# Kernel tuning notes

Measured on AMD Instinct MI355X. Metric: run time of the kernel, lower is better.

## Reference

```python
import jax, jax.numpy as jnp
import numpy as np

DIM = 8          # per-head dim
EPS = 1e-15
GROUPS_PW = 192  # 3 * heads = 3 * 64


def _conv(x, w, groups=1, pad=0):
    return jax.lax.conv_general_dilated(
        x, w, window_strides=(1, 1), padding=[(pad, pad), (pad, pad)],
        dimension_numbers=('NCHW', 'OIHW', 'NCHW'), feature_group_count=groups)


def setup_inputs() -> dict:
    key = jax.random.key(0)
    k0, k1, k2, k3, k4 = jax.random.split(key, 5)
    B, C, H, W = 4, 512, 64, 64
    td = 512  # heads * dim
    x = jax.random.normal(k0, (B, C, H, W), jnp.float32)
    w_qkv = jax.random.normal(k1, (3 * td, C, 1, 1), jnp.float32) * 0.05
    w_dw = jax.random.normal(k2, (3 * td, 1, 5, 5), jnp.float32) * 0.05
    w_pw = jax.random.normal(k3, (3 * td, (3 * td) // GROUPS_PW, 1, 1), jnp.float32) * 0.05
    w_proj = jax.random.normal(k4, (C, 2 * td, 1, 1), jnp.float32) * 0.05
    return {'x': x, 'w_qkv': w_qkv, 'w_dw': w_dw, 'w_pw': w_pw, 'w_proj': w_proj}


def reference(x, w_qkv, w_dw, w_pw, w_proj):
    # qkv projection (1x1 conv, no bias, no norm/act per config)
    qkv = _conv(x, w_qkv)  # [B, 3*td, H, W]
    # multi-scale aggregation: depthwise 5x5 then grouped 1x1 (groups = 3*heads)
    agg = _conv(_conv(qkv, w_dw, groups=w_dw.shape[0], pad=2), w_pw, groups=GROUPS_PW)
    qkv = jnp.concatenate([qkv, agg], axis=1)  # [B, 6*td, H, W]

    B, _, H, W = qkv.shape
    qkv = qkv.reshape(B, -1, 3 * DIM, H * W)  # [B, h_eff, 3*dim, HW]
    q = jax.nn.relu(qkv[:, :, :DIM])          # [B, h, dim, HW]
    k = jax.nn.relu(qkv[:, :, DIM:2 * DIM])   # [B, h, dim, HW]
    v = qkv[:, :, 2 * DIM:]                   # [B, h, dim, HW]
    # pad v with a row of ones -> normalization trick
    v = jnp.pad(v, ((0, 0), (0, 0), (0, 1), (0, 0)), constant_values=1.0)
    # linear attention via associativity: (v k^T) q
    vk = jnp.einsum('bhdn,bhen->bhde', v, k)   # [B, h, dim+1, dim]
    out = jnp.einsum('bhde,bhen->bhdn', vk, q) # [B, h, dim+1, HW]
    out = out[:, :, :-1] / (out[:, :, -1:] + EPS)
    out = out.reshape(B, -1, H, W)             # [B, 2*td, H, W]
    return x + _conv(out, w_proj)
```

## Files before the change

kernel.cpp:

```cpp
#include <hip/hip_runtime.h>
#include <hip/hip_bf16.h>
#include <cstdint>
#include <cstddef>


typedef __hip_bfloat16 bf16;
typedef __attribute__((ext_vector_type(8))) short short8;
typedef __attribute__((ext_vector_type(4))) float f32x4;

__device__ __forceinline__ float b2f(bf16 v) { return __bfloat162float(v); }
__device__ __forceinline__ bf16 f2b(float v) { return __float2bfloat16(v); }
__device__ __forceinline__ float us2f(unsigned short u) {
    return __uint_as_float(((unsigned)u) << 16);
}

__device__ __forceinline__ float dot2bf(unsigned p, unsigned wp, float acc) {
#if __has_builtin(__builtin_amdgcn_fdot2_f32_bf16)
    typedef __attribute__((ext_vector_type(2))) __bf16 bf16x2;
    return __builtin_amdgcn_fdot2_f32_bf16(
        __builtin_bit_cast(bf16x2, p), __builtin_bit_cast(bf16x2, wp),
        acc, false);
#else
    return acc
        + us2f((unsigned short)(p & 0xffffu))  * us2f((unsigned short)(wp & 0xffffu))
        + us2f((unsigned short)(p >> 16))      * us2f((unsigned short)(wp >> 16));
#endif
}

__device__ __forceinline__ void async16(void* lds_base, const void* gaddr) {
    __builtin_amdgcn_global_load_lds(
        (const __attribute__((address_space(1))) unsigned int*)gaddr,
        (__attribute__((address_space(3))) unsigned int*)lds_base,
        16, 0, 0);
}

__global__ __launch_bounds__(256) void convert_kernel(
    const float* __restrict__ src, bf16* __restrict__ dst, int n)
{
    int i = blockIdx.x * 256 + threadIdx.x;
    if (i < n) dst[i] = f2b(src[i]);
}

__global__ __launch_bounds__(256) void transpose_x_kernel(
    const float* __restrict__ x, bf16* __restrict__ x_t)
{
    __shared__ bf16 tile[32][33];
    const int b = blockIdx.z;
    const int c0 = blockIdx.y * 32;
    const int n0 = blockIdx.x * 32;
    const int tx = threadIdx.x & 31, ty = threadIdx.x >> 5;
    #pragma unroll
    for (int i = 0; i < 32; i += 8)
        tile[ty + i][tx] = f2b(x[((size_t)b * 512 + c0 + ty + i) * 4096 + n0 + tx]);
    __syncthreads();
    #pragma unroll
    for (int i = 0; i < 32; i += 8)
        x_t[((size_t)b * 4096 + n0 + ty + i) * 512 + c0 + tx] = tile[tx][ty + i];
}

template <bool PROJ>
__global__ __launch_bounds__(256) void mfma_gemm_kernel(
    const bf16* __restrict__ A, const bf16* __restrict__ xt_or_qkv,
    const bf16* __restrict__ agg, const float* __restrict__ X,
    void* __restrict__ Cout, int M, int K)
{
    constexpr int N = 4096;
    const int b = blockIdx.z;
    const int m_blk = blockIdx.y * 128;
    const int n_blk = blockIdx.x * 128;

    __shared__ short As[2][128 * 32];
    __shared__ short Bs[2][128 * 32];

    const int tid = threadIdx.x;
    const int lane = tid & 63, wave = tid >> 6;
    const int wm = (wave >> 1) * 64, wn = (wave & 1) * 64;
    const int fm = lane & 15, fq = lane >> 4;

    f32x4 acc[4][4] = {};

    const short* Ag = (const short*)A;
    const short* Btg = PROJ ? nullptr
        : (const short*)(xt_or_qkv + (size_t)b * N * 512);

    auto stage = [&](int buf, int k0) {
        #pragma unroll
        for (int t0 = 0; t0 < 2; ++t0) {
            int t = wave + t0 * 4;
            int row = m_blk + t * 16 + (lane >> 2);
            int col = k0 + (lane & 3) * 8;
            async16(&As[buf][t * 512], Ag + (size_t)row * K + col);
        }
        #pragma unroll
        for (int t0 = 0; t0 < 2; ++t0) {
            int t = wave + t0 * 4;
            int n = n_blk + t * 16 + (lane >> 2);
            if (!PROJ) {
                int col = k0 + (lane & 3) * 8;
                async16(&Bs[buf][t * 512], Btg + (size_t)n * 512 + col);
            } else {
                int h = (k0 >> 3) + (lane & 3);
                const bf16* chunk = (h < 64 ? xt_or_qkv : agg) +
                    ((size_t)b * 1536 + (size_t)(h & 63) * 24 + 16) * 4096;
                async16(&Bs[buf][t * 512], chunk + (size_t)n * 8);
            }
        }
    };

    stage(0, 0);
    asm volatile("s_waitcnt vmcnt(0)" ::: "memory");
    __builtin_amdgcn_s_barrier();

    int cur = 0;
    for (int k0 = 32; k0 <= K; k0 += 32) {
        if (k0 < K) stage(cur ^ 1, k0);

        short8 af[4], bfv[4];
        #pragma unroll
        for (int i = 0; i < 4; ++i)
            af[i] = *(const short8*)&As[cur][(wm + i * 16 + fm) * 32 + fq * 8];
        #pragma unroll
        for (int j = 0; j < 4; ++j)
            bfv[j] = *(const short8*)&Bs[cur][(wn + j * 16 + fm) * 32 + fq * 8];
        #pragma unroll
        for (int i = 0; i < 4; ++i)
            #pragma unroll
            for (int j = 0; j < 4; ++j)
                acc[i][j] = __builtin_amdgcn_mfma_f32_16x16x32_bf16(
                    af[i], bfv[j], acc[i][j], 0, 0, 0);

        asm volatile("s_waitcnt vmcnt(0)" ::: "memory");
        __builtin_amdgcn_s_barrier();
        cur ^= 1;
    }

    if (!PROJ) {
        bf16* Cb = (bf16*)Cout + (size_t)b * M * N;
        #pragma unroll
        for (int i = 0; i < 4; ++i)
            #pragma unroll
            for (int j = 0; j < 4; ++j) {
                int n = n_blk + wn + j * 16 + fm;
                #pragma unroll
                for (int r = 0; r < 4; ++r) {
                    int m = m_blk + wm + i * 16 + fq * 4 + r;
                    Cb[(size_t)m * N + n] = f2b(acc[i][j][r]);
                }
            }
    } else {
        float* Ob = (float*)Cout + (size_t)b * M * N;
        const float* Xb = X + (size_t)b * M * N;
        #pragma unroll
        for (int i = 0; i < 4; ++i)
            #pragma unroll
            for (int j = 0; j < 4; ++j) {
                int n = n_blk + wn + j * 16 + fm;
                #pragma unroll
                for (int r = 0; r < 4; ++r) {
                    int m = m_blk + wm + i * 16 + fq * 4 + r;
                    size_t off = (size_t)m * N + n;
                    Ob[off] = acc[i][j][r] + Xb[off];
                }
            }
    }
}

__global__ __launch_bounds__(256) void dwpw_kernel(
    const bf16* __restrict__ qkv, const float* __restrict__ w_dw,
    const float* __restrict__ w_pw, bf16* __restrict__ agg)
{
    const int bg = blockIdx.y;
    const int b = bg / 192;
    const int g = bg - b * 192;
    const int y0 = blockIdx.x * 32;

    __shared__ unsigned s_wdwp[8][16];
    __shared__ float s_wpw[8][8];

    const int tid = threadIdx.x;

    if (tid < 120) {
        int c = tid / 15, s = tid - c * 15;
        int i = s / 3, p = s - i * 3;
        int idx = i * 5 + p * 2;
        float w0 = w_dw[(size_t)(g * 8 + c) * 25 + idx];
        float w1 = (p < 2) ? w_dw[(size_t)(g * 8 + c) * 25 + idx + 1] : 0.f;
        unsigned u0 = __builtin_bit_cast(unsigned short, f2b(w0));
        unsigned u1 = __builtin_bit_cast(unsigned short, f2b(w1));
        s_wdwp[c][s] = u0 | (u1 << 16);
    }
    if (tid < 64)
        s_wpw[tid >> 3][tid & 7] = w_pw[(size_t)(g * 8 + (tid >> 3)) * 8 + (tid & 7)];
    __syncthreads();

    const int py = tid >> 3;
    const int sx = tid & 7;
    const int yq = y0 + py;
    const size_t chan_base = ((size_t)b * 1536 + g * 8) * 4096;

    const unsigned lo_keep = (sx > 0) ? 0xFFFFFFFFu : 0u;
    const unsigned hi_keep = (sx < 7) ? 0xFFFFFFFFu : 0u;

    float dwv[8][8];
    #pragma unroll
    for (int c = 0; c < 8; ++c) {
        unsigned wpq[16];
        #pragma unroll
        for (int q = 0; q < 4; ++q)
            *(uint4*)&wpq[q * 4] = *(const uint4*)&s_wdwp[c][q * 4];

        const char* cbase = (const char*)(qkv + chan_base + (size_t)c * 4096);
        float a[8] = {};
        #pragma unroll
        for (int i = 0; i < 5; ++i) {
            const int y = yq + i - 2;
            const bool row_ok = ((unsigned)y < 64u);
            const int yc = row_ok ? y : 0;
            const char* rowp = cbase + yc * 128;
            uint4 mid = *(const uint4*)(rowp + 16 * sx);
            const unsigned m = row_ok ? 0xFFFFFFFFu : 0u;

            unsigned lo = (unsigned)__shfl_up((int)mid.w, 1, 64);
            unsigned hi = (unsigned)__shfl_down((int)mid.x, 1, 64);

            unsigned W0 = lo & m & lo_keep;
            unsigned W1 = mid.x & m, W2 = mid.y & m;
            unsigned W3 = mid.z & m, W4 = mid.w & m;
            unsigned W5 = hi & m & hi_keep;
            unsigned S0 = __builtin_amdgcn_alignbit(W1, W0, 16);
            unsigned S1 = __builtin_amdgcn_alignbit(W2, W1, 16);
            unsigned S2 = __builtin_amdgcn_alignbit(W3, W2, 16);
            unsigned S3 = __builtin_amdgcn_alignbit(W4, W3, 16);
            unsigned S4 = __builtin_amdgcn_alignbit(W5, W4, 16);
            unsigned S5 = W5 >> 16;

            unsigned w01 = wpq[i * 3], w23 = wpq[i * 3 + 1], w4z = wpq[i * 3 + 2];
            a[0] = dot2bf(W0, w01, dot2bf(W1, w23, dot2bf(W2, w4z, a[0])));
            a[2] = dot2bf(W1, w01, dot2bf(W2, w23, dot2bf(W3, w4z, a[2])));
            a[4] = dot2bf(W2, w01, dot2bf(W3, w23, dot2bf(W4, w4z, a[4])));
            a[6] = dot2bf(W3, w01, dot2bf(W4, w23, dot2bf(W5, w4z, a[6])));
            a[1] = dot2bf(S0, w01, dot2bf(S1, w23, dot2bf(S2, w4z, a[1])));
            a[3] = dot2bf(S1, w01, dot2bf(S2, w23, dot2bf(S3, w4z, a[3])));
            a[5] = dot2bf(S2, w01, dot2bf(S3, w23, dot2bf(S4, w4z, a[5])));
            a[7] = dot2bf(S3, w01, dot2bf(S4, w23, dot2bf(S5, w4z, a[7])));
        }
        #pragma unroll
        for (int x = 0; x < 8; ++x) dwv[c][x] = a[x];
    }

    const size_t out_pix = (size_t)yq * 64 + 8 * sx;
    #pragma unroll
    for (int o = 0; o < 8; ++o) {
        float wv[8];
        *(float4*)&wv[0] = *(const float4*)&s_wpw[o][0];
        *(float4*)&wv[4] = *(const float4*)&s_wpw[o][4];
        float s[8] = {};
        #pragma unroll
        for (int i = 0; i < 8; ++i)
            #pragma unroll
            for (int x = 0; x < 8; ++x) s[x] += dwv[i][x] * wv[i];
        union { bf16 hv[8]; uint4 u; } pk;
        #pragma unroll
        for (int x = 0; x < 8; ++x) pk.hv[x] = f2b(s[x]);
        *(uint4*)(agg + chan_base + (size_t)o * 4096 + out_pix) = pk.u;
    }
}

__global__ __launch_bounds__(512) void vk_kernel(
    const bf16* __restrict__ qkv, const bf16* __restrict__ agg,
    float* __restrict__ vk)
{
    const int bh = blockIdx.x;
    const int b = bh >> 7;
    const int h = bh & 127;
    const bf16* base = (h < 64)
        ? (qkv + ((size_t)b * 1536 + h * 24) * 4096)
        : (agg + ((size_t)b * 1536 + (h - 64) * 24) * 4096);

    const int tid = threadIdx.x;
    const int n0 = tid * 8;

    short8 kr[8], vr[8];
    #pragma unroll
    for (int e = 0; e < 8; ++e)
        kr[e] = *(const short8*)&base[(size_t)(8 + e) * 4096 + n0];
    #pragma unroll
    for (int d = 0; d < 8; ++d)
        vr[d] = *(const short8*)&base[(size_t)(16 + d) * 4096 + n0];

    float acc[9][8] = {};
    #pragma unroll
    for (int t = 0; t < 8; ++t) {
        float kt[8], vt[8];
        #pragma unroll
        for (int e = 0; e < 8; ++e)
            kt[e] = fmaxf(us2f((unsigned short)kr[e][t]), 0.f);
        #pragma unroll
        for (int d = 0; d < 8; ++d)
            vt[d] = us2f((unsigned short)vr[d][t]);
        #pragma unroll
        for (int d = 0; d < 8; ++d)
            #pragma unroll
            for (int e = 0; e < 8; ++e)
                acc[d][e] += vt[d] * kt[e];
        #pragma unroll
        for (int e = 0; e < 8; ++e) acc[8][e] += kt[e];
    }

    __shared__ float red[8][72];
    const int lane = tid & 63, wave = tid >> 6;
    #pragma unroll
    for (int d = 0; d < 9; ++d) {
        #pragma unroll
        for (int e = 0; e < 8; ++e) {
            float v = acc[d][e];
            #pragma unroll
            for (int off = 32; off > 0; off >>= 1) v += __shfl_down(v, off, 64);
            if (lane == 0) red[wave][d * 8 + e] = v;
        }
    }
    __syncthreads();
    if (tid < 72) {
        float v = 0.f;
        #pragma unroll
        for (int w = 0; w < 8; ++w) v += red[w][tid];
        vk[(size_t)bh * 72 + tid] = v;
    }
}

__global__ __launch_bounds__(256) void attn_out_kernel(
    bf16* __restrict__ qkv, bf16* __restrict__ agg,
    const float* __restrict__ vk)
{
    const int b = blockIdx.z;
    const int h = blockIdx.y;
    const int n0 = (blockIdx.x * 256 + threadIdx.x) * 8;
    bf16* base = (h < 64)
        ? (qkv + ((size_t)b * 1536 + h * 24) * 4096)
        : (agg + ((size_t)b * 1536 + (h - 64) * 24) * 4096);

    __shared__ float s_vk[72];
    if (threadIdx.x < 72)
        s_vk[threadIdx.x] = vk[((size_t)b * 128 + h) * 72 + threadIdx.x];
    __syncthreads();

    short8 qr[8];
    #pragma unroll
    for (int e = 0; e < 8; ++e)
        qr[e] = *(const short8*)&base[(size_t)e * 4096 + n0];

    char* outp = (char*)(base + (size_t)16 * 4096) + (size_t)n0 * 16;
    #pragma unroll
    for (int t = 0; t < 8; ++t) {
        float q[8];
        #pragma unroll
        for (int e = 0; e < 8; ++e)
            q[e] = fmaxf(us2f((unsigned short)qr[e][t]), 0.f);

        float o[9];
        #pragma unroll
        for (int d = 0; d < 9; ++d) {
            float s = 0.f;
            #pragma unroll
            for (int e = 0; e < 8; ++e) s += s_vk[d * 8 + e] * q[e];
            o[d] = s;
        }
        const float denom = o[8] + 1e-15f;

        union { bf16 hv[8]; uint4 u; } pk;
        #pragma unroll
        for (int d = 0; d < 8; ++d) pk.hv[d] = f2b(o[d] / denom);
        *(uint4*)(outp + (size_t)t * 16) = pk.u;
    }
}

extern "C" void kernel_launch(void* const* d_in, const int* in_sizes, int n_in,
                              void* d_out, int out_size, void* d_ws, size_t ws_size,
                              hipStream_t stream) {
    const float* x      = (const float*)d_in[0];
    const float* w_qkv  = (const float*)d_in[1];
    const float* w_dw   = (const float*)d_in[2];
    const float* w_pw   = (const float*)d_in[3];
    const float* w_proj = (const float*)d_in[4];

    char* ws = (char*)d_ws;
    bf16* w_qkv_bf  = (bf16*)ws;
    bf16* w_proj_bf = (bf16*)(ws + 1572864);
    float* vkbf     = (float*)(ws + 1572864 + 1048576);
    bf16* x_t       = (bf16*)(ws + 1572864 + 1048576 + 147456);
    bf16* qkv       = x_t + (size_t)4 * 4096 * 512;
    bf16* agg       = qkv + (size_t)4 * 1536 * 4096;

    convert_kernel<<<3072, 256, 0, stream>>>(w_qkv, w_qkv_bf, 786432);
    convert_kernel<<<2048, 256, 0, stream>>>(w_proj, w_proj_bf, 524288);
    transpose_x_kernel<<<dim3(128, 16, 4), 256, 0, stream>>>(x, x_t);

    mfma_gemm_kernel<false><<<dim3(32, 12, 4), 256, 0, stream>>>(
        w_qkv_bf, x_t, nullptr, nullptr, qkv, 1536, 512);

    dwpw_kernel<<<dim3(2, 768), 256, 0, stream>>>(qkv, w_dw, w_pw, agg);

    vk_kernel<<<dim3(512), 512, 0, stream>>>(qkv, agg, vkbf);

    attn_out_kernel<<<dim3(2, 128, 4), 256, 0, stream>>>(qkv, agg, vkbf);

    mfma_gemm_kernel<true><<<dim3(32, 4, 4), 256, 0, stream>>>(
        w_proj_bf, qkv, agg, x, d_out, 512, 1024);
}
```

Measured before the change: 248.8 us.

## Use 64-row GEMM tiles with triple-buffered async loads

Both MFMA GEMMs now use a 64x128 output tile instead of 128x128, which doubles the grid in the M dimension, and switch from double to triple buffering. Two stages are prefetched ahead, with a partial vmcnt wait so loads overlap compute. The goal is more blocks for occupancy across CUs and better latency hiding of global loads. The cost is more B-tile reloads per output and less MFMA work per LDS load.

```diff
diff --git a/kernel.cpp b/kernel.cpp
--- a/kernel.cpp
+++ b/kernel.cpp
@@ -65,31 +65,30 @@
     void* __restrict__ Cout, int M, int K)
 {
     constexpr int N = 4096;
+    constexpr int BM = 64;
     const int b = blockIdx.z;
-    const int m_blk = blockIdx.y * 128;
+    const int m_blk = blockIdx.y * BM;
     const int n_blk = blockIdx.x * 128;
 
-    __shared__ short As[2][128 * 32];
-    __shared__ short Bs[2][128 * 32];
+    __shared__ short As[3][BM * 32];
+    __shared__ short Bs[3][128 * 32];
 
     const int tid = threadIdx.x;
     const int lane = tid & 63, wave = tid >> 6;
-    const int wm = (wave >> 1) * 64, wn = (wave & 1) * 64;
+    const int wm = (wave >> 1) * 32, wn = (wave & 1) * 64;
     const int fm = lane & 15, fq = lane >> 4;
 
-    f32x4 acc[4][4] = {};
+    f32x4 acc[2][4] = {};
 
     const short* Ag = (const short*)A;
     const short* Btg = PROJ ? nullptr
         : (const short*)(xt_or_qkv + (size_t)b * N * 512);
 
     auto stage = [&](int buf, int k0) {
-        #pragma unroll
-        for (int t0 = 0; t0 < 2; ++t0) {
-            int t = wave + t0 * 4;
-            int row = m_blk + t * 16 + (lane >> 2);
+        {
+            int row = m_blk + wave * 16 + (lane >> 2);
             int col = k0 + (lane & 3) * 8;
-            async16(&As[buf][t * 512], Ag + (size_t)row * K + col);
+            async16(&As[buf][wave * 512], Ag + (size_t)row * K + col);
         }
         #pragma unroll
         for (int t0 = 0; t0 < 2; ++t0) {
@@ -107,37 +106,46 @@
         }
     };
 
+    const int nt = K >> 5;
     stage(0, 0);
-    asm volatile("s_waitcnt vmcnt(0)" ::: "memory");
-    __builtin_amdgcn_s_barrier();
-
-    int cur = 0;
-    for (int k0 = 32; k0 <= K; k0 += 32) {
-        if (k0 < K) stage(cur ^ 1, k0);
-
-        short8 af[4], bfv[4];
-        #pragma unroll
-        for (int i = 0; i < 4; ++i)
-            af[i] = *(const short8*)&As[cur][(wm + i * 16 + fm) * 32 + fq * 8];
+    stage(1, 32);
+
+    int cb = 0;
+    int sb = 2;
+    for (int t = 0; t < nt; ++t) {
+        if (t + 2 < nt) {
+            stage(sb, (t + 2) * 32);
+            asm volatile("s_waitcnt vmcnt(6)" ::: "memory");
+        } else if (t + 1 < nt) {
+            asm volatile("s_waitcnt vmcnt(3)" ::: "memory");
+        } else {
+            asm volatile("s_waitcnt vmcnt(0)" ::: "memory");
+        }
+        __builtin_amdgcn_s_barrier();
+
+        short8 af[2], bfv[4];
+        #pragma unroll
+        for (int i = 0; i < 2; ++i)
+            af[i] = *(const short8*)&As[cb][(wm + i * 16 + fm) * 32 + fq * 8];
         #pragma unroll
         for (int j = 0; j < 4; ++j)
-            bfv[j] = *(const short8*)&Bs[cur][(wn + j * 16 + fm) * 32 + fq * 8];
-        #pragma unroll
-        for (int i = 0; i < 4; ++i)
+            bfv[j] = *(const short8*)&Bs[cb][(wn + j * 16 + fm) * 32 + fq * 8];
+        #pragma unroll
+        for (int i = 0; i < 2; ++i)
             #pragma unroll
             for (int j = 0; j < 4; ++j)
                 acc[i][j] = __builtin_amdgcn_mfma_f32_16x16x32_bf16(
                     af[i], bfv[j], acc[i][j], 0, 0, 0);
 
-        asm volatile("s_waitcnt vmcnt(0)" ::: "memory");
         __builtin_amdgcn_s_barrier();
-        cur ^= 1;
+        cb = (cb == 2) ? 0 : cb + 1;
+        sb = (sb == 2) ? 0 : sb + 1;
     }
 
     if (!PROJ) {
         bf16* Cb = (bf16*)Cout + (size_t)b * M * N;
         #pragma unroll
-        for (int i = 0; i < 4; ++i)
+        for (int i = 0; i < 2; ++i)
             #pragma unroll
             for (int j = 0; j < 4; ++j) {
                 int n = n_blk + wn + j * 16 + fm;
@@ -151,7 +159,7 @@
         float* Ob = (float*)Cout + (size_t)b * M * N;
         const float* Xb = X + (size_t)b * M * N;
         #pragma unroll
-        for (int i = 0; i < 4; ++i)
+        for (int i = 0; i < 2; ++i)
             #pragma unroll
             for (int j = 0; j < 4; ++j) {
                 int n = n_blk + wn + j * 16 + fm;
@@ -395,7 +403,7 @@
     convert_kernel<<<2048, 256, 0, stream>>>(w_proj, w_proj_bf, 524288);
     transpose_x_kernel<<<dim3(128, 16, 4), 256, 0, stream>>>(x, x_t);
 
-    mfma_gemm_kernel<false><<<dim3(32, 12, 4), 256, 0, stream>>>(
+    mfma_gemm_kernel<false><<<dim3(32, 24, 4), 256, 0, stream>>>(
         w_qkv_bf, x_t, nullptr, nullptr, qkv, 1536, 512);
 
     dwpw_kernel<<<dim3(2, 768), 256, 0, stream>>>(qkv, w_dw, w_pw, agg);
@@ -404,6 +412,6 @@
 
     attn_out_kernel<<<dim3(2, 128, 4), 256, 0, stream>>>(qkv, agg, vkbf);
 
-    mfma_gemm_kernel<true><<<dim3(32, 4, 4), 256, 0, stream>>>(
+    mfma_gemm_kernel<true><<<dim3(32, 8, 4), 256, 0, stream>>>(
         w_proj_bf, qkv, agg, x, d_out, 512, 1024);
 }
```

Measured after the change: 258.6 us. 3.9% more time.
